# Kernel tuning notes

Hardware: AMD Instinct MI355X
Metric: run time of the kernel (lower is better)

## Reference

```python
import jax, jax.numpy as jnp
import numpy as np

B, CIN, COUT, GC, H, W = 8, 64, 64, 64, 320, 320
K = 3      # guided conv kernel size
P = 1      # padding
KGL = 3    # kernel-generation layer kernel size
LEAK = 0.2
EPS = 1e-5


def setup_inputs() -> dict:
    key = jax.random.key(0)
    ks = jax.random.split(key, 4)
    return {
        "data": jax.random.normal(ks[0], (B, CIN, H, W), jnp.float32),
        "guidance": jax.random.normal(ks[1], (B, GC, H, W), jnp.float32),
        "w_kgl": jax.random.normal(ks[2], (CIN, GC, KGL, KGL), jnp.float32) * 0.02,
        "b_kgl": jnp.zeros((CIN,), jnp.float32),
        "w_cc": jax.random.normal(ks[3], (CIN * COUT, GC), jnp.float32) * 0.02,
        "b_cc": jnp.zeros((CIN * COUT,), jnp.float32),
        "gamma": jnp.ones((COUT,), jnp.float32),
        "beta": jnp.zeros((COUT,), jnp.float32),
    }


def reference(data, guidance, w_kgl, b_kgl, w_cc, b_cc, gamma, beta):
    pad = P + KGL // 2  # = 2, so kernel map is [B, CIN, H+2P, W+2P]
    kernel = jax.lax.conv_general_dilated(
        guidance, w_kgl, window_strides=(1, 1),
        padding=[(pad, pad), (pad, pad)],
        dimension_numbers=("NCHW", "OIHW", "NCHW"),
    ) + b_kgl[None, :, None, None]

    # channel-wise guided conv: zero-pad input, multiply per-pixel kernel map,
    # then box-sum over KxK windows (== conv with an all-ones KxK kernel)
    xp = jnp.pad(data, ((0, 0), (0, 0), (P, P), (P, P)))  # [B,CIN,H+2P,W+2P]
    prod = xp * kernel
    x1 = jax.lax.reduce_window(prod, 0.0, jax.lax.add,
                               (1, 1, K, K), (1, 1, 1, 1), "VALID")  # [B,CIN,H,W]

    # cross-channel: per-frame 1x1 conv generated from mean guidance intensity
    mean_g = guidance.mean(axis=(2, 3))                       # [B, GC]
    kcc = (mean_g @ w_cc.T + b_cc).reshape(B, COUT, CIN)      # [B, Cout, Cin]
    x2 = jnp.einsum("bchw,boc->bohw", x1, kcc)                # [B, Cout, H, W]

    x3 = jnp.where(x2 > 0, x2, LEAK * x2)  # leaky relu

    # batchnorm (training-mode statistics over B,H,W per channel)
    mu = x3.mean(axis=(0, 2, 3), keepdims=True)
    var = x3.var(axis=(0, 2, 3), keepdims=True)
    xn = (x3 - mu) * jax.lax.rsqrt(var + EPS)
    return xn * gamma[None, :, None, None] + beta[None, :, None, None]
```

## Files before the change

kernel.cpp:

```cpp
#include <hip/hip_runtime.h>

#define BB 8
#define CINC 64
#define COUTC 64
#define GCC 64
#define HH 320
#define WW 320
#define HP 322
#define WP 322
#define LEAK 0.2f
#define EPSB 1e-5f
#define HWSZ (HH*WW)
#define HWPSZ (HP*WP)

typedef unsigned short u16;
typedef __attribute__((ext_vector_type(8))) short short8v;
typedef __attribute__((ext_vector_type(16))) float f32x16;
typedef __attribute__((ext_vector_type(4))) unsigned int u32x4;

static __device__ __forceinline__ u16 f2bf(float f) {
    unsigned u = __float_as_uint(f);
    u += 0x7fffu + ((u >> 16) & 1u);
    return (u16)(u >> 16);
}
static __device__ __forceinline__ unsigned pk2bf(float a, float b) {
    return (unsigned)f2bf(a) | ((unsigned)f2bf(b) << 16);
}
static __device__ __forceinline__ unsigned swzA(int cc) {
    return (unsigned)((((cc >> 1) & 1) << 5) | (((cc >> 2) & 1) << 4));
}

__global__ __launch_bounds__(256) void k_mean(const float* __restrict__ g,
                                              float* __restrict__ mean_g) {
    int row = blockIdx.x;
    const float4* p = (const float4*)(g + (size_t)row * HWSZ);
    float s = 0.f;
    for (int i = threadIdx.x; i < HWSZ / 4; i += 256) {
        float4 v = p[i];
        s += v.x + v.y + v.z + v.w;
    }
    #pragma unroll
    for (int off = 32; off; off >>= 1) s += __shfl_down(s, off);
    __shared__ float ls[4];
    if ((threadIdx.x & 63) == 0) ls[threadIdx.x >> 6] = s;
    __syncthreads();
    if (threadIdx.x == 0)
        mean_g[row] = (ls[0] + ls[1] + ls[2] + ls[3]) * (1.f / (float)HWSZ);
}

__global__ __launch_bounds__(256) void k_kcc(const float* __restrict__ mean_g,
                                             const float* __restrict__ w_cc,
                                             const float* __restrict__ b_cc,
                                             u16* __restrict__ kccB) {
    int idx = blockIdx.x * 256 + threadIdx.x;
    if (idx >= BB * COUTC * CINC) return;
    int b = idx >> 12;
    int j = idx & 4095;
    const float* mg = mean_g + b * GCC;
    const float* wr = w_cc + (size_t)j * GCC;
    float s = b_cc[j];
    #pragma unroll
    for (int g = 0; g < GCC; ++g) s += mg[g] * wr[g];
    kccB[idx] = f2bf(s);
}

__global__ __launch_bounds__(256) void k_wb(const float* __restrict__ w_kgl,
                                            u16* __restrict__ wB) {
    int idx = blockIdx.x * 256 + threadIdx.x;
    if (idx >= 36864) return;
    int j   = idx & 7;
    int lhi = (idx >> 3) & 1;
    int l   = (idx >> 4) & 31;
    int nj  = (idx >> 9) & 1;
    int t   = idx >> 10;
    int tap = t % 9, gk = t / 9;
    int ks = gk & 1, gc = gk >> 1;
    int cout = nj * 32 + l;
    int g = gc * 32 + ks * 16 + lhi * 8 + j;
    wB[idx] = f2bf(w_kgl[((size_t)(cout * 64 + g)) * 9 + tap]);
}

__global__ __launch_bounds__(256) void k_trc(const float* __restrict__ data,
                                             u16* __restrict__ dataC, int b0) {
    int w0 = blockIdx.x * 64;
    int h  = blockIdx.y;
    int bi = blockIdx.z;
    int bg = b0 + bi;
    int tid = threadIdx.x;
    __shared__ u16 tile[64][68];
    const float* src = data + ((size_t)bg * CINC) * HWSZ + (size_t)h * WW + w0;
    #pragma unroll
    for (int k = 0; k < 4; ++k) {
        int i = tid + k * 256;
        int c = i >> 4, wq = i & 15;
        float4 v = *(const float4*)(src + (size_t)c * HWSZ + wq * 4);
        tile[c][wq * 4 + 0] = f2bf(v.x);
        tile[c][wq * 4 + 1] = f2bf(v.y);
        tile[c][wq * 4 + 2] = f2bf(v.z);
        tile[c][wq * 4 + 3] = f2bf(v.w);
    }
    __syncthreads();
    u16* dst = dataC + (size_t)bi * HWSZ * CINC;
    #pragma unroll
    for (int k = 0; k < 2; ++k) {
        int i = tid + k * 256;
        int w = i >> 3, g8 = i & 7;
        union { u16 s[8]; u32x4 v; } t;
        #pragma unroll
        for (int j = 0; j < 8; ++j) t.s[j] = tile[g8 * 8 + j][w];
        size_t px = (size_t)h * WW + w0 + w;
        *(u32x4*)(dst + ((size_t)(g8 >> 1) * HWSZ + px) * 16 + (g8 & 1) * 8) = t.v;
    }
}

__global__ __launch_bounds__(384) void k_convm(const float* __restrict__ guid,
                                               const u16* __restrict__ wB,
                                               const float* __restrict__ b_kgl,
                                               u16* __restrict__ ker, int b0) {
    int xt = blockIdx.x, rt = blockIdx.y, bi = blockIdx.z;
    int bg = b0 + bi;
    int tid = threadIdx.x;
    int x0 = xt * 64, oy0 = rt * 6;
    __shared__ __align__(16) u16 ldsA[8 * 66 * 32];
    __shared__ __align__(16) u16 ldsB[9 * 2 * 32 * 16];

    int wv = tid >> 6, lane = tid & 63;
    int l31 = lane & 31, lhi = lane >> 5;
    f32x16 acc[2][2] = {};

    for (int gc = 0; gc < 2; ++gc) {
        for (int ks = 0; ks < 2; ++ks) {
            if (gc | ks) __syncthreads();
            const u16* bsrc = wB + (gc * 2 + ks) * 9216;
            #pragma unroll
            for (int k = 0; k < 3; ++k) {
                int i = tid + k * 384;
                *(u32x4*)(ldsB + (size_t)i * 8) = *(const u32x4*)(bsrc + (size_t)i * 8);
            }
            if (ks == 0) {
                const float* gbase = guid + ((size_t)bg * 64 + gc * 32) * HWSZ;
                for (int i = tid; i < 544; i += 384) {
                    int qa = i % 17;
                    int rem = i / 17;
                    int go = rem & 3, rr = rem >> 2;
                    int iy = oy0 - 2 + rr;
                    int ix0 = x0 - 4 + 4 * qa;
                    union { float4 q; float f[4]; } va[8];
                    bool rowok = (iy >= 0) & (iy < HH);
                    if (rowok & (ix0 >= 0) & (ix0 + 3 < WW)) {
                        #pragma unroll
                        for (int j = 0; j < 8; ++j)
                            va[j].q = *(const float4*)(gbase + (size_t)(go * 8 + j) * HWSZ
                                                       + (size_t)iy * WW + ix0);
                    } else {
                        #pragma unroll
                        for (int j = 0; j < 8; ++j)
                            #pragma unroll
                            for (int t = 0; t < 4; ++t) {
                                int ix = ix0 + t;
                                va[j].f[t] = (rowok & (ix >= 0) & (ix < WW))
                                    ? gbase[(size_t)(go * 8 + j) * HWSZ + (size_t)iy * WW + ix]
                                    : 0.f;
                            }
                    }
                    #pragma unroll
                    for (int t = 0; t < 4; ++t) {
                        int cc = 4 * qa - 2 + t;
                        if (cc >= 0 && cc < 66) {
                            u32x4 wvv;
                            wvv[0] = pk2bf(va[0].f[t], va[1].f[t]);
                            wvv[1] = pk2bf(va[2].f[t], va[3].f[t]);
                            wvv[2] = pk2bf(va[4].f[t], va[5].f[t]);
                            wvv[3] = pk2bf(va[6].f[t], va[7].f[t]);
                            unsigned off = ((unsigned)((rr * 66 + cc) * 4 + go) * 16u)
                                           ^ swzA(cc);
                            *(u32x4*)((char*)ldsA + off) = wvv;
                        }
                    }
                }
            }
            __syncthreads();

            for (int tap = 0; tap < 9; ++tap) {
                int di = tap / 3, dj = tap - di * 3;
                short8v Bf[2];
                #pragma unroll
                for (int nj = 0; nj < 2; ++nj)
                    Bf[nj] = *(const short8v*)(ldsB +
                        (((size_t)tap * 2 + nj) * 32 + l31) * 16 + lhi * 8);
                int rrow = wv + di;
                #pragma unroll
                for (int s = 0; s < 2; ++s) {
                    int cc = s * 32 + l31 + dj;
                    unsigned off = ((unsigned)((rrow * 66 + cc) * 4 + ks * 2 + lhi) * 16u)
                                   ^ swzA(cc);
                    short8v a = *(const short8v*)((const char*)ldsA + off);
                    acc[s][0] = __builtin_amdgcn_mfma_f32_32x32x16_bf16(a, Bf[0], acc[s][0], 0, 0, 0);
                    acc[s][1] = __builtin_amdgcn_mfma_f32_32x32x16_bf16(a, Bf[1], acc[s][1], 0, 0, 0);
                }
            }
        }
    }

    int oy = oy0 + wv;
    if (oy < HP) {
        float bias0 = b_kgl[l31], bias1 = b_kgl[32 + l31];
        u16* kout = ker + (size_t)bi * HWPSZ * GCC;
        int ckl = l31 >> 4, idx = l31 & 15;
        #pragma unroll
        for (int s = 0; s < 2; ++s)
            #pragma unroll
            for (int r = 0; r < 16; ++r) {
                int pxc = x0 + s * 32 + (r & 3) + 8 * (r >> 2) + 4 * lhi;
                if (pxc < WP) {
                    size_t pix = (size_t)oy * WP + pxc;
                    kout[((size_t)ckl * HWPSZ + pix) * 16 + idx]       = f2bf(acc[s][0][r] + bias0);
                    kout[((size_t)(2 + ckl) * HWPSZ + pix) * 16 + idx] = f2bf(acc[s][1][r] + bias1);
                }
            }
    }
}

__global__ __launch_bounds__(384) void k_mix(const u16* __restrict__ dataC,
                                             const u16* __restrict__ ker,
                                             const u16* __restrict__ kccB,
                                             float* __restrict__ out,
                                             float* __restrict__ stats, int b0) {
    int xt = blockIdx.x, rt = blockIdx.y, bi = blockIdx.z;
    int b = b0 + bi;
    int w0 = xt * 64, oy0 = rt * 6;
    int tid = threadIdx.x, wv = tid >> 6, lane = tid & 63;
    int l31 = lane & 31, lhi = lane >> 5;

    __shared__ __align__(16) float prd[2 * 528 * 8];
    __shared__ float bsum[64], bsq[64];

    if (tid < 64) { bsum[tid] = 0.f; bsq[tid] = 0.f; }

    const u16* kerb = ker + (size_t)bi * HWPSZ * GCC;
    const u16* datb = dataC + (size_t)bi * HWSZ * CINC;
    const u16* kcb  = kccB + (size_t)b * COUTC * CINC;

    f32x16 acc[2][2] = {};

    for (int ck = 0; ck < 4; ++ck) {
        if (ck) __syncthreads();
        #pragma unroll
        for (int t = tid; t < 1056; t += 384) {
            int c2 = t & 1, px = t >> 1;
            int r = px / 66, cc = px - r * 66;
            int u = oy0 + r, kcol = w0 + cc;
            int iu = u - 1, iv = kcol - 1;
            float pr[8];
            if (u < HP && iu >= 0 && iu < HH && iv >= 0 && iv < WW) {
                u32x4 kv = *(const u32x4*)(kerb + ((size_t)ck * HWPSZ + (size_t)u * WP + kcol) * 16 + c2 * 8);
                u32x4 dv = *(const u32x4*)(datb + ((size_t)ck * HWSZ + (size_t)iu * WW + iv) * 16 + c2 * 8);
                const unsigned* kw = (const unsigned*)&kv;
                const unsigned* dw = (const unsigned*)&dv;
                #pragma unroll
                for (int p = 0; p < 4; ++p) {
                    pr[2 * p]     = __uint_as_float(kw[p] << 16) * __uint_as_float(dw[p] << 16);
                    pr[2 * p + 1] = __uint_as_float(kw[p] & 0xffff0000u) * __uint_as_float(dw[p] & 0xffff0000u);
                }
            } else {
                #pragma unroll
                for (int j = 0; j < 8; ++j) pr[j] = 0.f;
            }
            float* pp = prd + c2 * 4224 + px * 8;
            *(float4*)pp       = make_float4(pr[0], pr[1], pr[2], pr[3]);
            *(float4*)(pp + 4) = make_float4(pr[4], pr[5], pr[6], pr[7]);
        }
        __syncthreads();

        short8v ka0 = *(const short8v*)(kcb + ((size_t)l31 * 64 + ck * 16 + lhi * 8));
        short8v ka1 = *(const short8v*)(kcb + ((size_t)(32 + l31) * 64 + ck * 16 + lhi * 8));

        #pragma unroll
        for (int s = 0; s < 2; ++s) {
            float x1v[8];
            #pragma unroll
            for (int j = 0; j < 8; ++j) x1v[j] = 0.f;
            #pragma unroll
            for (int di = 0; di < 3; ++di) {
                int row = wv + di;
                #pragma unroll
                for (int dj = 0; dj < 3; ++dj) {
                    int col = s * 32 + l31 + dj;
                    const float* pp = prd + lhi * 4224 + (row * 66 + col) * 8;
                    float4 a0 = *(const float4*)pp;
                    float4 a1 = *(const float4*)(pp + 4);
                    x1v[0] += a0.x; x1v[1] += a0.y; x1v[2] += a0.z; x1v[3] += a0.w;
                    x1v[4] += a1.x; x1v[5] += a1.y; x1v[6] += a1.z; x1v[7] += a1.w;
                }
            }
            union { u16 h[8]; short8v v8; } xb;
            #pragma unroll
            for (int j = 0; j < 8; ++j) xb.h[j] = f2bf(x1v[j]);
            acc[0][s] = __builtin_amdgcn_mfma_f32_32x32x16_bf16(ka0, xb.v8, acc[0][s], 0, 0, 0);
            acc[1][s] = __builtin_amdgcn_mfma_f32_32x32x16_bf16(ka1, xb.v8, acc[1][s], 0, 0, 0);
        }
    }

    int oy = oy0 + wv;
    if (oy < HH) {
        #pragma unroll
        for (int nj = 0; nj < 2; ++nj)
            #pragma unroll
            for (int r = 0; r < 16; ++r) {
                int o = nj * 32 + (r & 3) + 8 * (r >> 2) + 4 * lhi;
                float v0 = acc[nj][0][r]; v0 = v0 > 0.f ? v0 : LEAK * v0;
                float v1 = acc[nj][1][r]; v1 = v1 > 0.f ? v1 : LEAK * v1;
                size_t rowb = ((size_t)(b * COUTC + o)) * HWSZ + (size_t)oy * WW + w0;
                out[rowb + l31]      = v0;
                out[rowb + 32 + l31] = v1;
                float ss = v0 + v1, qq = v0 * v0 + v1 * v1;
                #pragma unroll
                for (int off = 16; off; off >>= 1) {
                    ss += __shfl_xor(ss, off);
                    qq += __shfl_xor(qq, off);
                }
                if (l31 == 0) { atomicAdd(&bsum[o], ss); atomicAdd(&bsq[o], qq); }
            }
    }
    __syncthreads();
    int rep = (blockIdx.x + blockIdx.y * 5 + blockIdx.z * 3) & 7;
    if (tid < 64) {
        atomicAdd(&stats[rep * 128 + tid], bsum[tid]);
        atomicAdd(&stats[rep * 128 + 64 + tid], bsq[tid]);
    }
}

__global__ void k_fin(const float* __restrict__ stats,
                      const float* __restrict__ gamma, const float* __restrict__ beta,
                      float* __restrict__ scale, float* __restrict__ shift) {
    int o = threadIdx.x;
    float s = 0.f, q = 0.f;
    #pragma unroll
    for (int r = 0; r < 8; ++r) { s += stats[r * 128 + o]; q += stats[r * 128 + 64 + o]; }
    float n = (float)BB * (float)HWSZ;
    float mu = s / n;
    float var = q / n - mu * mu;
    float rs = rsqrtf(var + EPSB);
    float sc = rs * gamma[o];
    scale[o] = sc;
    shift[o] = beta[o] - mu * sc;
}

__global__ __launch_bounds__(256) void k_norm(float* __restrict__ x,
                                              const float* __restrict__ scale,
                                              const float* __restrict__ shift) {
    size_t i = (size_t)blockIdx.x * 256 + threadIdx.x;
    int ch = (int)((i * 4) / HWSZ) & 63;
    float4 v = ((float4*)x)[i];
    float sc = scale[ch], sh = shift[ch];
    v.x = v.x * sc + sh; v.y = v.y * sc + sh; v.z = v.z * sc + sh; v.w = v.w * sc + sh;
    ((float4*)x)[i] = v;
}

extern "C" void kernel_launch(void* const* d_in, const int* in_sizes, int n_in,
                              void* d_out, int out_size, void* d_ws, size_t ws_size,
                              hipStream_t stream) {
    const float* data  = (const float*)d_in[0];
    const float* guid  = (const float*)d_in[1];
    const float* w_kgl = (const float*)d_in[2];
    const float* b_kgl = (const float*)d_in[3];
    const float* w_cc  = (const float*)d_in[4];
    const float* b_cc  = (const float*)d_in[5];
    const float* gamma = (const float*)d_in[6];
    const float* beta  = (const float*)d_in[7];
    float* out = (float*)d_out;
    float* ws  = (float*)d_ws;

    float* mean_g = ws;
    float* stats  = ws + 512;
    float* scale  = stats + 1024;
    float* shift  = scale + 64;
    u16*   kccB   = (u16*)(ws + 1664);
    u16*   wB     = kccB + BB * 4096;
    u16*   dataC  = wB + 36864;

    size_t used_us = 1664 * 2 + BB * 4096 + 36864;
    size_t cap_us  = (ws_size / 2 > used_us) ? ws_size / 2 - used_us : 0;
    size_t per_b   = (size_t)GCC * (HWSZ + HWPSZ);
    int bs = 4;
    while (bs > 1 && (size_t)bs * per_b > cap_us) bs >>= 1;
    u16* kerC = dataC + (size_t)bs * HWSZ * GCC;

    hipMemsetAsync(stats, 0, 1024 * sizeof(float), stream);
    k_mean<<<BB * GCC, 256, 0, stream>>>(guid, mean_g);
    k_kcc<<<(BB * COUTC * CINC + 255) / 256, 256, 0, stream>>>(mean_g, w_cc, b_cc, kccB);
    k_wb<<<144, 256, 0, stream>>>(w_kgl, wB);

    for (int b0 = 0; b0 < BB; b0 += bs) {
        int nb = (BB - b0 < bs) ? BB - b0 : bs;
        k_trc<<<dim3(WW / 64, HH, nb), 256, 0, stream>>>(data, dataC, b0);
        k_convm<<<dim3(6, 54, nb), 384, 0, stream>>>(guid, wB, b_kgl, kerC, b0);
        k_mix<<<dim3(5, 54, nb), 384, 0, stream>>>(dataC, kerC, kccB, out, stats, b0);
    }
    k_fin<<<1, 64, 0, stream>>>(stats, gamma, beta, scale, shift);
    k_norm<<<(out_size / 4 + 255) / 256, 256, 0, stream>>>(out, scale, shift);
}
```

Before: 645.3 us.

## Prefetch next channel chunk into registers and swizzle LDS product tile

The fused guided-conv/MFMA kernel now issues the global loads for the next 16-channel chunk into registers right after the barrier, so they are in flight while the current chunk's box-sum and MFMAs run. It also XOR-swizzles the LDS product buffer addresses by pixel index to reduce bank conflicts on the strided float4 reads and writes. The cost is higher register pressure from holding six 128-bit vectors per thread, which could lower occupancy.

```diff
diff --git a/kernel.cpp b/kernel.cpp
--- a/kernel.cpp
+++ b/kernel.cpp
@@ -28,6 +28,9 @@
 }
 static __device__ __forceinline__ unsigned swzA(int cc) {
     return (unsigned)((((cc >> 1) & 1) << 5) | (((cc >> 2) & 1) << 4));
+}
+static __device__ __forceinline__ unsigned swzP(int px) {
+    return ((unsigned)(px >> 2) & 7u) << 4;
 }
 
 __global__ __launch_bounds__(256) void k_mean(const float* __restrict__ g,
@@ -242,35 +245,52 @@
     const u16* kcb  = kccB + (size_t)b * COUTC * CINC;
 
     f32x16 acc[2][2] = {};
-
+    u32x4 kvr[3], dvr[3];
+
+#define MIX_LOAD(CK)                                                          \
+    {                                                                         \
+        _Pragma("unroll")                                                     \
+        for (int it = 0; it < 3; ++it) {                                      \
+            int t = tid + it * 384;                                           \
+            if (t < 1056) {                                                   \
+                int c2 = t & 1, px = t >> 1;                                  \
+                int r = px / 66, cc = px - r * 66;                            \
+                int u = oy0 + r, kcol = w0 + cc;                              \
+                int iu = u - 1, iv = kcol - 1;                                \
+                u32x4 kz = {0, 0, 0, 0}, dz = {0, 0, 0, 0};                   \
+                if (u < HP && iu >= 0 && iu < HH && iv >= 0 && iv < WW) {     \
+                    kz = *(const u32x4*)(kerb + ((size_t)(CK) * HWPSZ + (size_t)u * WP + kcol) * 16 + c2 * 8); \
+                    dz = *(const u32x4*)(datb + ((size_t)(CK) * HWSZ + (size_t)iu * WW + iv) * 16 + c2 * 8);   \
+                }                                                             \
+                kvr[it] = kz; dvr[it] = dz;                                   \
+            }                                                                 \
+        }                                                                     \
+    }
+
+    MIX_LOAD(0);
+
+    #pragma unroll
     for (int ck = 0; ck < 4; ++ck) {
         if (ck) __syncthreads();
         #pragma unroll
-        for (int t = tid; t < 1056; t += 384) {
-            int c2 = t & 1, px = t >> 1;
-            int r = px / 66, cc = px - r * 66;
-            int u = oy0 + r, kcol = w0 + cc;
-            int iu = u - 1, iv = kcol - 1;
-            float pr[8];
-            if (u < HP && iu >= 0 && iu < HH && iv >= 0 && iv < WW) {
-                u32x4 kv = *(const u32x4*)(kerb + ((size_t)ck * HWPSZ + (size_t)u * WP + kcol) * 16 + c2 * 8);
-                u32x4 dv = *(const u32x4*)(datb + ((size_t)ck * HWSZ + (size_t)iu * WW + iv) * 16 + c2 * 8);
-                const unsigned* kw = (const unsigned*)&kv;
-                const unsigned* dw = (const unsigned*)&dv;
+        for (int it = 0; it < 3; ++it) {
+            int t = tid + it * 384;
+            if (t < 1056) {
+                int c2 = t & 1, px = t >> 1;
+                float pr[8];
                 #pragma unroll
                 for (int p = 0; p < 4; ++p) {
-                    pr[2 * p]     = __uint_as_float(kw[p] << 16) * __uint_as_float(dw[p] << 16);
-                    pr[2 * p + 1] = __uint_as_float(kw[p] & 0xffff0000u) * __uint_as_float(dw[p] & 0xffff0000u);
-                }
-            } else {
-                #pragma unroll
-                for (int j = 0; j < 8; ++j) pr[j] = 0.f;
-            }
-            float* pp = prd + c2 * 4224 + px * 8;
-            *(float4*)pp       = make_float4(pr[0], pr[1], pr[2], pr[3]);
-            *(float4*)(pp + 4) = make_float4(pr[4], pr[5], pr[6], pr[7]);
+                    pr[2 * p]     = __uint_as_float(kvr[it][p] << 16) * __uint_as_float(dvr[it][p] << 16);
+                    pr[2 * p + 1] = __uint_as_float(kvr[it][p] & 0xffff0000u) * __uint_as_float(dvr[it][p] & 0xffff0000u);
+                }
+                unsigned fo = (unsigned)((c2 * 4224 + px * 8) * 4);
+                unsigned x = swzP(px);
+                *(float4*)((char*)prd + (fo ^ x))        = make_float4(pr[0], pr[1], pr[2], pr[3]);
+                *(float4*)((char*)prd + ((fo + 16) ^ x)) = make_float4(pr[4], pr[5], pr[6], pr[7]);
+            }
         }
         __syncthreads();
+        if (ck < 3) MIX_LOAD(ck + 1);
 
         short8v ka0 = *(const short8v*)(kcb + ((size_t)l31 * 64 + ck * 16 + lhi * 8));
         short8v ka1 = *(const short8v*)(kcb + ((size_t)(32 + l31) * 64 + ck * 16 + lhi * 8));
@@ -286,9 +306,11 @@
                 #pragma unroll
                 for (int dj = 0; dj < 3; ++dj) {
                     int col = s * 32 + l31 + dj;
-                    const float* pp = prd + lhi * 4224 + (row * 66 + col) * 8;
-                    float4 a0 = *(const float4*)pp;
-                    float4 a1 = *(const float4*)(pp + 4);
+                    int px = row * 66 + col;
+                    unsigned fo = (unsigned)((lhi * 4224 + px * 8) * 4);
+                    unsigned x = swzP(px);
+                    float4 a0 = *(const float4*)((const char*)prd + (fo ^ x));
+                    float4 a1 = *(const float4*)((const char*)prd + ((fo + 16) ^ x));
                     x1v[0] += a0.x; x1v[1] += a0.y; x1v[2] += a0.z; x1v[3] += a0.w;
                     x1v[4] += a1.x; x1v[5] += a1.y; x1v[6] += a1.z; x1v[7] += a1.w;
                 }
@@ -300,6 +322,7 @@
             acc[1][s] = __builtin_amdgcn_mfma_f32_32x32x16_bf16(ka1, xb.v8, acc[1][s], 0, 0, 0);
         }
     }
+#undef MIX_LOAD
 
     int oy = oy0 + wv;
     if (oy < HH) {
```

New measurement: 604.1 us. 6.4% less time.
